# Performance work log

Measured on AMD Instinct MI355X. Metric: run time of the kernel, lower is better.

Reference implementation:

```python
import jax, jax.numpy as jnp
import numpy as np

SEQ, DM, NH, DH = 8192, 1024, 16, 64


def setup_inputs() -> dict:
    key = jax.random.key(0)
    k = jax.random.split(key, 8)
    return {
        "xs": jax.random.normal(k[0], (SEQ, DM), dtype=jnp.float32),
        "wq": jax.random.normal(k[1], (NH, DH, DM), dtype=jnp.float32),
        "wk": jax.random.normal(k[2], (NH, DH, DM), dtype=jnp.float32),
        "wv": jax.random.normal(k[3], (NH, DH, DM), dtype=jnp.float32),
        # MLP: Linear(NH*DH -> DM), gelu, Linear(DM -> NH*DH); eqx stores W as (out, in)
        "w1": jax.random.normal(k[4], (DM, NH * DH), dtype=jnp.float32) * 0.02,
        "b1": jnp.zeros((DM,), dtype=jnp.float32),
        "w2": jax.random.normal(k[5], (NH * DH, DM), dtype=jnp.float32) * 0.02,
        "b2": jnp.zeros((NH * DH,), dtype=jnp.float32),
    }


def _act(x):
    return jax.nn.elu(x) + 1.0


def reference(xs, wq, wk, wv, w1, b1, w2, b2):
    # project: (n_heads d_head d_model),(seq d_model) -> (seq n_heads d_head)
    q = jnp.einsum('hdm,sm->shd', wq, xs)
    k = jnp.einsum('hdm,sm->shd', wk, xs)
    v = jnp.einsum('hdm,sm->shd', wv, xs)

    def cell(state, qkv):
        s, z = state                      # s: (h, dk, dv), z: (h, dk)
        qt, kt, vt = qkv                  # each (h, d)
        kt = _act(kt)
        s = s + jnp.einsum('hk,hv->hkv', kt, vt)
        z = z + kt
        qa = _act(qt)
        # faithful to einops 'n_heads d_head_k d_head_v, n_heads d_head_q -> n_heads d_head_v'
        sq = jnp.einsum('hkv,hq->hv', s, qa)
        zq = jnp.einsum('hk,hq->h', z, qa)
        return (s, z), sq / zq[:, None]

    init = (jnp.zeros((NH, DH, DH), xs.dtype), jnp.zeros((NH, DH), xs.dtype))
    _, out = jax.lax.scan(cell, init, (q, k, v))   # out: (seq, h, d)
    out = out.reshape(SEQ, NH * DH)
    h = jax.nn.gelu(out @ w1.T + b1)
    return h @ w2.T + b2
```

## Files before the change

### kernel.cpp

```cpp
#include <hip/hip_runtime.h>
#include <hip/hip_bf16.h>

using bf16 = __hip_bfloat16;
typedef __attribute__((ext_vector_type(8))) short shortx8;
typedef __attribute__((ext_vector_type(4))) float f32x4;

#define SEQ 8192
#define DM 1024
#define NH 16
#define CHUNK 64
#define NC (SEQ / CHUNK)

__device__ __forceinline__ void load_lds16(const bf16* g, bf16* l) {
    __builtin_amdgcn_global_load_lds(
        (const __attribute__((address_space(1))) void*)g,
        (__attribute__((address_space(3))) void*)l, 16, 0, 0);
}

__device__ __forceinline__ float bf2f(short s) {
    union { unsigned u; float f; } x;
    x.u = ((unsigned)(unsigned short)s) << 16;
    return x.f;
}

#define XS_G ((size_t)SEQ * DM / 4)
#define W_G  ((size_t)DM * DM / 4)
__global__ __launch_bounds__(256) void convert_all(const float* __restrict__ xs,
                                                   const float* __restrict__ wk,
                                                   const float* __restrict__ wv,
                                                   const float* __restrict__ w1,
                                                   const float* __restrict__ w2,
                                                   bf16* __restrict__ xsb,
                                                   bf16* __restrict__ wall) {
    size_t g = (size_t)blockIdx.x * 256 + threadIdx.x;
    const float* in;
    bf16* out;
    size_t off;
    if (g < XS_G) {
        in = xs; out = xsb; off = g;
    } else {
        size_t r = g - XS_G;
        int w = (int)(r / W_G);
        off = r % W_G;
        const float* ws[4] = {wk, wv, w1, w2};
        in = ws[w];
        out = wall + (size_t)w * DM * DM / 4 * 4;
    }
    size_t i = off * 4;
    float4 f = *(const float4*)(in + i);
    out[i + 0] = __float2bfloat16(f.x);
    out[i + 1] = __float2bfloat16(f.y);
    out[i + 2] = __float2bfloat16(f.z);
    out[i + 3] = __float2bfloat16(f.w);
}

template <int MODE>
__global__ __launch_bounds__(256) void gemm_nt(const bf16* __restrict__ A,
                                               const bf16* __restrict__ B,
                                               void* __restrict__ Cv,
                                               const float* __restrict__ bias,
                                               float* __restrict__ kappa,
                                               float* __restrict__ numbuf,
                                               float* __restrict__ denbuf,
                                               int M, int N, int K) {
    __shared__ bf16 As[128][64];
    __shared__ bf16 Bs[128][64];
    __shared__ float Ksh[4][64];

    const int tid  = threadIdx.x;
    const int L    = blockIdx.x + blockIdx.y * gridDim.x;
    const int ry   = L % gridDim.y;
    const int rx   = L / gridDim.y;
    const int bm   = ry * 128;
    const int bn   = rx * 128;
    const int wave = tid >> 6;
    const int lane = tid & 63;
    const int wm   = (wave >> 1) * 64;
    const int wn   = (wave & 1) * 64;
    const int quad = lane >> 4;
    const int m16  = lane & 15;
    const int r7   = m16 & 7;

    f32x4 acc[4][4];
    #pragma unroll
    for (int i = 0; i < 4; ++i)
        #pragma unroll
        for (int j = 0; j < 4; ++j)
            #pragma unroll
            for (int r = 0; r < 4; ++r) acc[i][j][r] = 0.f;

    for (int k0 = 0; k0 < K; k0 += 64) {
        #pragma unroll
        for (int it = 0; it < 4; ++it) {
            int s = it * 256 + tid;
            int row = s >> 3, pos = s & 7;
            int g = pos ^ (row & 7);
            load_lds16(A + (size_t)(bm + row) * K + k0 + g * 8, &As[row][pos * 8]);
            load_lds16(B + (size_t)(bn + row) * K + k0 + g * 8, &Bs[row][pos * 8]);
        }
        __syncthreads();

        #pragma unroll
        for (int kx = 0; kx < 2; ++kx) {
            const int p = ((kx << 2) + quad) ^ r7;
            shortx8 af[4], bfr[4];
            #pragma unroll
            for (int i = 0; i < 4; ++i)
                af[i] = *(const shortx8*)&As[wm + i * 16 + m16][p * 8];
            #pragma unroll
            for (int j = 0; j < 4; ++j)
                bfr[j] = *(const shortx8*)&Bs[wn + j * 16 + m16][p * 8];
            #pragma unroll
            for (int i = 0; i < 4; ++i)
                #pragma unroll
                for (int j = 0; j < 4; ++j)
                    acc[i][j] = __builtin_amdgcn_mfma_f32_16x16x32_bf16(af[i], bfr[j], acc[i][j], 0, 0, 0);
        }
        __syncthreads();
    }

    if (MODE == 0) {
        const int h = (bn + wn) >> 6;
        #pragma unroll
        for (int i = 0; i < 4; ++i) {
            #pragma unroll
            for (int r = 0; r < 4; ++r) {
                float s = 0.f;
                #pragma unroll
                for (int j = 0; j < 4; ++j) {
                    float v = acc[i][j][r];
                    s += v > 0.f ? v + 1.f : __expf(v);
                }
                s += __shfl_xor(s, 1);
                s += __shfl_xor(s, 2);
                s += __shfl_xor(s, 4);
                s += __shfl_xor(s, 8);
                if (m16 == 0)
                    kappa[(size_t)h * SEQ + bm + wm + i * 16 + quad * 4 + r] = s;
            }
        }
        return;
    }

    if (MODE == 1) {
        const int c = (bm + wm) >> 6;
        const int h = (bn + wn) >> 6;
        float kv = kappa[(size_t)h * SEQ + bm + wm + lane];
        Ksh[wave][lane] = kv;
        float dsum = kv;
        #pragma unroll
        for (int off = 32; off > 0; off >>= 1) dsum += __shfl_xor(dsum, off);
        if (lane == 0) denbuf[(size_t)h * NC + c] = dsum;

        float s[4] = {0.f, 0.f, 0.f, 0.f};
        #pragma unroll
        for (int i = 0; i < 4; ++i) {
            #pragma unroll
            for (int r = 0; r < 4; ++r) {
                float kr = Ksh[wave][i * 16 + quad * 4 + r];
                #pragma unroll
                for (int j = 0; j < 4; ++j) s[j] += kr * acc[i][j][r];
            }
        }
        #pragma unroll
        for (int j = 0; j < 4; ++j) {
            s[j] += __shfl_xor(s[j], 16);
            s[j] += __shfl_xor(s[j], 32);
        }
        if (quad == 0) {
            size_t nb = ((size_t)h * NC + c) * 64;
            #pragma unroll
            for (int j = 0; j < 4; ++j) numbuf[nb + j * 16 + m16] = s[j];
        }
    }

    #pragma unroll
    for (int i = 0; i < 4; ++i) {
        int row0 = bm + wm + i * 16 + quad * 4;
        #pragma unroll
        for (int j = 0; j < 4; ++j) {
            int col = bn + wn + j * 16 + m16;
            #pragma unroll
            for (int r = 0; r < 4; ++r) {
                float v = acc[i][j][r];
                size_t o = (size_t)(row0 + r) * N + col;
                if (MODE == 1) {
                    ((bf16*)Cv)[o] = __float2bfloat16(v);
                } else if (MODE == 2) {
                    v += bias[col];
                    float t = tanhf(0.7978845608028654f * (v + 0.044715f * v * v * v));
                    ((bf16*)Cv)[o] = __float2bfloat16(0.5f * v * (1.f + t));
                } else {
                    v += bias[col];
                    ((float*)Cv)[o] = v;
                }
            }
        }
    }
}

__global__ __launch_bounds__(256) void prefix_state(float* __restrict__ numbuf,
                                                    float* __restrict__ denbuf) {
    const int h = blockIdx.x;
    const int wave = threadIdx.x >> 6;
    const int d = threadIdx.x & 63;
    __shared__ float tot[4][64];
    __shared__ float dtot[4];

    float val[32], dval[32];
    const int c0 = wave * 32;
    #pragma unroll
    for (int i = 0; i < 32; ++i) {
        size_t idx = (size_t)h * NC + c0 + i;
        val[i]  = numbuf[idx * 64 + d];
        dval[i] = denbuf[idx];
    }
    float run = 0.f, drun = 0.f;
    #pragma unroll
    for (int i = 0; i < 32; ++i) {
        float t = val[i];  val[i]  = run;  run  += t;
        float dt = dval[i]; dval[i] = drun; drun += dt;
    }
    tot[wave][d] = run;
    if (d == 0) dtot[wave] = drun;
    __syncthreads();
    float off = 0.f, doff = 0.f;
    for (int w = 0; w < wave; ++w) { off += tot[w][d]; doff += dtot[w]; }
    #pragma unroll
    for (int i = 0; i < 32; ++i) {
        size_t idx = (size_t)h * NC + c0 + i;
        numbuf[idx * 64 + d] = val[i] + off;
        if (d == 0) denbuf[idx] = dval[i] + doff;
    }
}

__global__ __launch_bounds__(256) void chunk_out(const bf16* __restrict__ vb,
                                                 const float* __restrict__ kappa,
                                                 const float* __restrict__ numbuf,
                                                 const float* __restrict__ denbuf,
                                                 bf16* __restrict__ out) {
    const int h = blockIdx.x, c = blockIdx.y;
    __shared__ float Ksh[64];
    __shared__ float Vs[64][64];
    const int tid = threadIdx.x;

    #pragma unroll
    for (int it = 0; it < 2; ++it) {
        int s = it * 256 + tid;
        int r = s >> 3, d8 = (s & 7) * 8;
        shortx8 raw = *(const shortx8*)(vb + (size_t)(c * 64 + r) * DM + h * 64 + d8);
        #pragma unroll
        for (int e = 0; e < 8; ++e) Vs[r][d8 + e] = bf2f(raw[e]);
    }
    if (tid < 64) Ksh[tid] = kappa[(size_t)h * SEQ + c * 64 + tid];
    __syncthreads();

    const int t  = tid >> 2;
    const int v0 = (tid & 3) << 4;
    const size_t bidx = (size_t)h * NC + c;

    float den = denbuf[bidx];
    float num[16];
    #pragma unroll
    for (int jj = 0; jj < 4; ++jj) {
        float4 n4 = *(const float4*)&numbuf[bidx * 64 + v0 + jj * 4];
        num[jj * 4 + 0] = n4.x; num[jj * 4 + 1] = n4.y;
        num[jj * 4 + 2] = n4.z; num[jj * 4 + 3] = n4.w;
    }

    for (int i = 0; i <= t; ++i) {
        float s = Ksh[i];
        den += s;
        #pragma unroll
        for (int jj = 0; jj < 4; ++jj) {
            float4 v4 = *(const float4*)&Vs[i][v0 + jj * 4];
            num[jj * 4 + 0] += s * v4.x; num[jj * 4 + 1] += s * v4.y;
            num[jj * 4 + 2] += s * v4.z; num[jj * 4 + 3] += s * v4.w;
        }
    }

    const float inv = 1.0f / den;
    size_t og = (size_t)(c * 64 + t) * DM + h * 64 + v0;
    #pragma unroll
    for (int j = 0; j < 16; ++j) out[og + j] = __float2bfloat16(num[j] * inv);
}

extern "C" void kernel_launch(void* const* d_in, const int* in_sizes, int n_in,
                              void* d_out, int out_size, void* d_ws, size_t ws_size,
                              hipStream_t stream) {
    const float* xs = (const float*)d_in[0];
    const float* wk = (const float*)d_in[2];
    const float* wv = (const float*)d_in[3];
    const float* w1 = (const float*)d_in[4];
    const float* b1 = (const float*)d_in[5];
    const float* w2 = (const float*)d_in[6];
    const float* b2 = (const float*)d_in[7];
    float* y = (float*)d_out;

    char* base = (char*)d_ws;
    size_t off = 0;
    auto alloc = [&](size_t b) -> char* {
        char* p = base + off;
        off += (b + 255) & ~(size_t)255;
        return p;
    };

    const size_t NMAT = (size_t)SEQ * DM;
    const size_t NW   = (size_t)DM * DM;
    bf16*  xsb    = (bf16*)alloc(NMAT * 2);
    bf16*  wall   = (bf16*)alloc(4 * NW * 2);
    bf16*  wkb    = wall;
    bf16*  wvb    = wall + NW;
    bf16*  w1b    = wall + 2 * NW;
    bf16*  w2b    = wall + 3 * NW;
    bf16*  vb     = (bf16*)alloc(NMAT * 2);
    float* kappa  = (float*)alloc((size_t)NH * SEQ * 4);
    float* numbuf = (float*)alloc((size_t)NH * NC * 64 * 4);
    float* denbuf = (float*)alloc((size_t)NH * NC * 4);
    bf16*  outb   = (bf16*)alloc(NMAT * 2);
    bf16*  hb     = (bf16*)alloc(NMAT * 2);

    {
        size_t total_g = XS_G + 4 * W_G;
        convert_all<<<(int)(total_g / 256), 256, 0, stream>>>(xs, wk, wv, w1, w2,
                                                              xsb, wall);
    }

    dim3 ggrid(DM / 128, SEQ / 128);
    gemm_nt<0><<<ggrid, 256, 0, stream>>>(xsb, wkb, nullptr, nullptr, kappa,
                                          nullptr, nullptr, SEQ, DM, DM);
    gemm_nt<1><<<ggrid, 256, 0, stream>>>(xsb, wvb, vb, nullptr, kappa,
                                          numbuf, denbuf, SEQ, DM, DM);

    prefix_state<<<NH, 256, 0, stream>>>(numbuf, denbuf);
    chunk_out<<<dim3(NH, NC), 256, 0, stream>>>(vb, kappa, numbuf, denbuf, outb);

    gemm_nt<2><<<ggrid, 256, 0, stream>>>(outb, w1b, hb, b1, nullptr,
                                          nullptr, nullptr, SEQ, DM, DM);
    gemm_nt<3><<<ggrid, 256, 0, stream>>>(hb, w2b, y, b2, nullptr,
                                          nullptr, nullptr, SEQ, DM, DM);
}
```

Measured before the change: 239.1 us.

## Fuse K and V projections into one wide GEMM, move chunk sums to separate kernel

The K and V projection GEMMs are merged into a single GEMM with N=2*DM over the contiguous wk/wv bf16 weights. Column tiles in the K half reduce to kappa, and tiles in the V half store bf16 V. This removes one launch and fills the grid better. Because kappa is no longer ready inside the V epilogue, the per-chunk numerator and denominator sums move into a new chunk_sums kernel that rereads V from memory, adding a launch and extra traffic.

```diff
diff --git a/kernel.cpp b/kernel.cpp
--- a/kernel.cpp
+++ b/kernel.cpp
@@ -44,7 +44,7 @@
         off = r % W_G;
         const float* ws[4] = {wk, wv, w1, w2};
         in = ws[w];
-        out = wall + (size_t)w * DM * DM / 4 * 4;
+        out = wall + (size_t)w * DM * DM;
     }
     size_t i = off * 4;
     float4 f = *(const float4*)(in + i);
@@ -60,12 +60,9 @@
                                                void* __restrict__ Cv,
                                                const float* __restrict__ bias,
                                                float* __restrict__ kappa,
-                                               float* __restrict__ numbuf,
-                                               float* __restrict__ denbuf,
                                                int M, int N, int K) {
     __shared__ bf16 As[128][64];
     __shared__ bf16 Bs[128][64];
-    __shared__ float Ksh[4][64];
 
     const int tid  = threadIdx.x;
     const int L    = blockIdx.x + blockIdx.y * gridDim.x;
@@ -120,58 +117,43 @@
     }
 
     if (MODE == 0) {
-        const int h = (bn + wn) >> 6;
-        #pragma unroll
-        for (int i = 0; i < 4; ++i) {
-            #pragma unroll
-            for (int r = 0; r < 4; ++r) {
-                float s = 0.f;
+        const int cbase = bn + wn;
+        if (cbase < DM) {
+            const int h = cbase >> 6;
+            #pragma unroll
+            for (int i = 0; i < 4; ++i) {
+                #pragma unroll
+                for (int r = 0; r < 4; ++r) {
+                    float s = 0.f;
+                    #pragma unroll
+                    for (int j = 0; j < 4; ++j) {
+                        float v = acc[i][j][r];
+                        s += v > 0.f ? v + 1.f : __expf(v);
+                    }
+                    s += __shfl_xor(s, 1);
+                    s += __shfl_xor(s, 2);
+                    s += __shfl_xor(s, 4);
+                    s += __shfl_xor(s, 8);
+                    if (m16 == 0)
+                        kappa[(size_t)h * SEQ + bm + wm + i * 16 + quad * 4 + r] = s;
+                }
+            }
+        } else {
+            const int col0 = cbase - DM;
+            #pragma unroll
+            for (int i = 0; i < 4; ++i) {
+                int row0 = bm + wm + i * 16 + quad * 4;
                 #pragma unroll
                 for (int j = 0; j < 4; ++j) {
-                    float v = acc[i][j][r];
-                    s += v > 0.f ? v + 1.f : __expf(v);
+                    int col = col0 + j * 16 + m16;
+                    #pragma unroll
+                    for (int r = 0; r < 4; ++r)
+                        ((bf16*)Cv)[(size_t)(row0 + r) * DM + col] =
+                            __float2bfloat16(acc[i][j][r]);
                 }
-                s += __shfl_xor(s, 1);
-                s += __shfl_xor(s, 2);
-                s += __shfl_xor(s, 4);
-                s += __shfl_xor(s, 8);
-                if (m16 == 0)
-                    kappa[(size_t)h * SEQ + bm + wm + i * 16 + quad * 4 + r] = s;
             }
         }
         return;
-    }
-
-    if (MODE == 1) {
-        const int c = (bm + wm) >> 6;
-        const int h = (bn + wn) >> 6;
-        float kv = kappa[(size_t)h * SEQ + bm + wm + lane];
-        Ksh[wave][lane] = kv;
-        float dsum = kv;
-        #pragma unroll
-        for (int off = 32; off > 0; off >>= 1) dsum += __shfl_xor(dsum, off);
-        if (lane == 0) denbuf[(size_t)h * NC + c] = dsum;
-
-        float s[4] = {0.f, 0.f, 0.f, 0.f};
-        #pragma unroll
-        for (int i = 0; i < 4; ++i) {
-            #pragma unroll
-            for (int r = 0; r < 4; ++r) {
-                float kr = Ksh[wave][i * 16 + quad * 4 + r];
-                #pragma unroll
-                for (int j = 0; j < 4; ++j) s[j] += kr * acc[i][j][r];
-            }
-        }
-        #pragma unroll
-        for (int j = 0; j < 4; ++j) {
-            s[j] += __shfl_xor(s[j], 16);
-            s[j] += __shfl_xor(s[j], 32);
-        }
-        if (quad == 0) {
-            size_t nb = ((size_t)h * NC + c) * 64;
-            #pragma unroll
-            for (int j = 0; j < 4; ++j) numbuf[nb + j * 16 + m16] = s[j];
-        }
     }
 
     #pragma unroll
@@ -184,9 +166,7 @@
             for (int r = 0; r < 4; ++r) {
                 float v = acc[i][j][r];
                 size_t o = (size_t)(row0 + r) * N + col;
-                if (MODE == 1) {
-                    ((bf16*)Cv)[o] = __float2bfloat16(v);
-                } else if (MODE == 2) {
+                if (MODE == 2) {
                     v += bias[col];
                     float t = tanhf(0.7978845608028654f * (v + 0.044715f * v * v * v));
                     ((bf16*)Cv)[o] = __float2bfloat16(0.5f * v * (1.f + t));
@@ -196,6 +176,39 @@
                 }
             }
         }
+    }
+}
+
+__global__ __launch_bounds__(256) void chunk_sums(const bf16* __restrict__ vb,
+                                                  const float* __restrict__ kappa,
+                                                  float* __restrict__ numbuf,
+                                                  float* __restrict__ denbuf) {
+    const int h = blockIdx.x, c = blockIdx.y;
+    __shared__ float Ksh[64];
+    __shared__ float part[4][64];
+    const int tid = threadIdx.x;
+
+    if (tid < 64) Ksh[tid] = kappa[(size_t)h * SEQ + c * 64 + tid];
+    __syncthreads();
+
+    const int d  = tid & 63;
+    const int tq = tid >> 6;
+    float acc = 0.f;
+    #pragma unroll
+    for (int tt = 0; tt < 16; ++tt) {
+        int t = tq * 16 + tt;
+        acc += Ksh[t] * bf2f(*(const short*)(vb + (size_t)(c * 64 + t) * DM + h * 64 + d));
+    }
+    part[tq][d] = acc;
+    __syncthreads();
+
+    if (tid < 64) {
+        float s = part[0][tid] + part[1][tid] + part[2][tid] + part[3][tid];
+        numbuf[((size_t)h * NC + c) * 64 + tid] = s;
+        float kv = Ksh[tid];
+        #pragma unroll
+        for (int off = 32; off > 0; off >>= 1) kv += __shfl_down(kv, off);
+        if (tid == 0) denbuf[(size_t)h * NC + c] = kv;
     }
 }
 
@@ -309,8 +322,6 @@
     const size_t NW   = (size_t)DM * DM;
     bf16*  xsb    = (bf16*)alloc(NMAT * 2);
     bf16*  wall   = (bf16*)alloc(4 * NW * 2);
-    bf16*  wkb    = wall;
-    bf16*  wvb    = wall + NW;
     bf16*  w1b    = wall + 2 * NW;
     bf16*  w2b    = wall + 3 * NW;
     bf16*  vb     = (bf16*)alloc(NMAT * 2);
@@ -326,17 +337,15 @@
                                                               xsb, wall);
     }
 
-    dim3 ggrid(DM / 128, SEQ / 128);
-    gemm_nt<0><<<ggrid, 256, 0, stream>>>(xsb, wkb, nullptr, nullptr, kappa,
-                                          nullptr, nullptr, SEQ, DM, DM);
-    gemm_nt<1><<<ggrid, 256, 0, stream>>>(xsb, wvb, vb, nullptr, kappa,
-                                          numbuf, denbuf, SEQ, DM, DM);
-
+    dim3 kvgrid(2 * DM / 128, SEQ / 128);
+    gemm_nt<0><<<kvgrid, 256, 0, stream>>>(xsb, wall, vb, nullptr, kappa,
+                                           SEQ, 2 * DM, DM);
+
+    chunk_sums<<<dim3(NH, NC), 256, 0, stream>>>(vb, kappa, numbuf, denbuf);
     prefix_state<<<NH, 256, 0, stream>>>(numbuf, denbuf);
     chunk_out<<<dim3(NH, NC), 256, 0, stream>>>(vb, kappa, numbuf, denbuf, outb);
 
-    gemm_nt<2><<<ggrid, 256, 0, stream>>>(outb, w1b, hb, b1, nullptr,
-                                          nullptr, nullptr, SEQ, DM, DM);
-    gemm_nt<3><<<ggrid, 256, 0, stream>>>(hb, w2b, y, b2, nullptr,
-                                          nullptr, nullptr, SEQ, DM, DM);
-}
+    dim3 ggrid(DM / 128, SEQ / 128);
+    gemm_nt<2><<<ggrid, 256, 0, stream>>>(outb, w1b, hb, b1, nullptr, SEQ, DM, DM);
+    gemm_nt<3><<<ggrid, 256, 0, stream>>>(hb, w2b, y, b2, nullptr, SEQ, DM, DM);
+}
```

Result: slower. 255.3 us (+6.8%).
